# Performance work log

Hardware: AMD Instinct MI355X
Metric: run time of the kernel (lower is better)

Reference implementation:

```python
import jax, jax.numpy as jnp
import numpy as np

N = 100000
D = 64
H = 4 * D  # 256
E = 1000000


def setup_inputs() -> dict:
    key = jax.random.key(0)
    ks = jax.random.split(key, 9)
    return {
        "loc_feat": jax.random.normal(ks[0], (N, D), dtype=jnp.float32),
        "geo_src": jax.random.randint(ks[1], (E,), 0, N),
        "geo_dst": jax.random.randint(ks[2], (E,), 0, N),
        "trans_src": jax.random.randint(ks[3], (E,), 0, N),
        "trans_dst": jax.random.randint(ks[4], (E,), 0, N),
        "trans_w": jax.random.uniform(ks[5], (E,), dtype=jnp.float32),
        "W1": jax.random.normal(ks[6], (D, H), dtype=jnp.float32) * (1.0 / np.sqrt(D)),
        "b1": jax.random.normal(ks[7], (H,), dtype=jnp.float32) * 0.01,
        "W2": jax.random.normal(ks[8], (H, 1), dtype=jnp.float32) * (1.0 / np.sqrt(H)),
    }


def reference(loc_feat, geo_src, geo_dst, trans_src, trans_dst, trans_w, W1, b1, W2):
    n = loc_feat.shape[0]
    # etype 'geo': copy_u + mean  -> segment mean of src features at dst
    geo_sum = jax.ops.segment_sum(loc_feat[geo_src], geo_dst, num_segments=n)
    cnt = jax.ops.segment_sum(jnp.ones(geo_src.shape[0], loc_feat.dtype), geo_dst, num_segments=n)
    geo = jnp.where(cnt[:, None] > 0, geo_sum / jnp.maximum(cnt, 1.0)[:, None], 0.0)
    # etype 'trans': u_mul_e + sum -> weighted segment sum
    trans = jax.ops.segment_sum(loc_feat[trans_src] * trans_w[:, None], trans_dst, num_segments=n)
    # semantic attention fuse over the two relation views
    z = jnp.stack([geo, trans], axis=1)          # [N, 2, D]
    h = jnp.tanh(jnp.einsum('nkd,dh->nkh', z, W1) + b1)  # [N, 2, H]
    w = jnp.einsum('nkh,ho->nko', h, W2).mean(0)  # [2, 1] (mean over nodes)
    beta = jax.nn.softmax(w, axis=0)              # [2, 1]
    return (beta[None, :, :] * z).sum(1)          # [N, D]
```

## Files before the change

kernel.cpp:

```cpp
#include <hip/hip_runtime.h>
#include <hip/hip_bf16.h>

#define N_NODES 100000
#define DIM 64
#define HID 256
#define E_EDGES 1000000
#define TWO_N (2 * N_NODES)
#define MLP_ROWBLOCKS (TWO_N / 64)

#define TILE 240
#define NBINS 417
#define CAP 3072
#define EPB 8192
#define GEO_BLOCKS 123

typedef short short8 __attribute__((ext_vector_type(8)));
typedef float f32x4 __attribute__((ext_vector_type(4)));
typedef unsigned short us4 __attribute__((ext_vector_type(4)));

__device__ __forceinline__ float tanh_fast(float x) {
    x = fminf(fmaxf(x, -15.0f), 15.0f);
    float e = __expf(2.0f * x);
    return (e - 1.0f) / (e + 1.0f);
}

__device__ __forceinline__ unsigned short f2bf(float x) {
    unsigned u = __float_as_uint(x);
    u = u + 0x7FFFu + ((u >> 16) & 1u);
    return (unsigned short)(u >> 16);
}

__device__ __forceinline__ float bf2f(unsigned short u) {
    return __uint_as_float(((unsigned)u) << 16);
}

__global__ void pack_feat_kernel(const float* __restrict__ feat,
                                 unsigned short* __restrict__ fb) {
    int i = blockIdx.x * 256 + threadIdx.x;
    float4 v = ((const float4*)feat)[i];
    us4 o;
    o[0] = f2bf(v.x); o[1] = f2bf(v.y); o[2] = f2bf(v.z); o[3] = f2bf(v.w);
    ((us4*)fb)[i] = o;
}

__global__ void bin_fill_kernel(const int* __restrict__ gs, const int* __restrict__ gd,
                                const int* __restrict__ ts, const int* __restrict__ td,
                                const float* __restrict__ tw,
                                int* __restrict__ gcount,
                                int* __restrict__ gbin, int2* __restrict__ tbin) {
    __shared__ int hist[NBINS];
    __shared__ int baseS[NBINS];
    __shared__ int cur[NBINS];
    int t = threadIdx.x;
    int blk = blockIdx.x;
    int rel = (blk >= GEO_BLOCKS) ? 1 : 0;
    int e0 = (rel ? blk - GEO_BLOCKS : blk) * EPB;
    const int* dstp = rel ? td : gd;
    const int* srcp = rel ? ts : gs;

    for (int i = t; i < NBINS; i += 256) { hist[i] = 0; cur[i] = 0; }
    __syncthreads();

    #pragma unroll
    for (int j = 0; j < EPB / 1024; ++j) {
        int idx = e0 + j * 1024 + 4 * t;
        if (idx + 3 < E_EDGES) {
            int4 v = *(const int4*)&dstp[idx];
            atomicAdd(&hist[v.x / TILE], 1);
            atomicAdd(&hist[v.y / TILE], 1);
            atomicAdd(&hist[v.z / TILE], 1);
            atomicAdd(&hist[v.w / TILE], 1);
        } else {
            for (int i2 = 0; i2 < 4; ++i2)
                if (idx + i2 < E_EDGES) atomicAdd(&hist[dstp[idx + i2] / TILE], 1);
        }
    }
    __syncthreads();

    for (int i = t; i < NBINS; i += 256) {
        int h = hist[i];
        baseS[i] = (h > 0) ? (i * CAP + atomicAdd(&gcount[rel * NBINS + i], h)) : 0;
    }
    __syncthreads();

    if (!rel) {
        #pragma unroll
        for (int j = 0; j < EPB / 1024; ++j) {
            int idx = e0 + j * 1024 + 4 * t;
            bool vec = (idx + 3 < E_EDGES);
            int4 dv, sv;
            if (vec) { dv = *(const int4*)&dstp[idx]; sv = *(const int4*)&srcp[idx]; }
            int dd[4] = {dv.x, dv.y, dv.z, dv.w};
            int ss[4] = {sv.x, sv.y, sv.z, sv.w};
            for (int i2 = 0; i2 < 4; ++i2) {
                if (!vec) {
                    if (idx + i2 >= E_EDGES) continue;
                    dd[i2] = dstp[idx + i2]; ss[i2] = srcp[idx + i2];
                }
                int d = dd[i2];
                int bin = d / TILE;
                int pos = atomicAdd(&cur[bin], 1);
                int gi = baseS[bin] + pos;
                if (gi < (bin + 1) * CAP)
                    gbin[gi] = ss[i2] | ((d - bin * TILE) << 20);
            }
        }
    } else {
        #pragma unroll
        for (int j = 0; j < EPB / 1024; ++j) {
            int idx = e0 + j * 1024 + 4 * t;
            bool vec = (idx + 3 < E_EDGES);
            int4 dv, sv; float4 wv;
            if (vec) {
                dv = *(const int4*)&dstp[idx];
                sv = *(const int4*)&srcp[idx];
                wv = *(const float4*)&tw[idx];
            }
            int dd[4] = {dv.x, dv.y, dv.z, dv.w};
            int ss[4] = {sv.x, sv.y, sv.z, sv.w};
            float ww[4] = {wv.x, wv.y, wv.z, wv.w};
            for (int i2 = 0; i2 < 4; ++i2) {
                if (!vec) {
                    if (idx + i2 >= E_EDGES) continue;
                    dd[i2] = dstp[idx + i2]; ss[i2] = srcp[idx + i2]; ww[i2] = tw[idx + i2];
                }
                int d = dd[i2];
                int bin = d / TILE;
                int pos = atomicAdd(&cur[bin], 1);
                int gi = baseS[bin] + pos;
                if (gi < (bin + 1) * CAP)
                    tbin[gi] = make_int2(ss[i2] | ((d - bin * TILE) << 20),
                                         __float_as_int(ww[i2]));
            }
        }
    }
}

__global__ void __launch_bounds__(512) aggregate_kernel(
        const unsigned short* __restrict__ featb,
        const int* __restrict__ gbin, const int2* __restrict__ tbin,
        const int* __restrict__ gcount,
        unsigned short* __restrict__ zb) {
    __shared__ int   srcS[CAP];
    __shared__ float wS[CAP];
    __shared__ int   histS[TILE];
    __shared__ int   baseS[TILE];
    __shared__ int   curS[TILE];
    __shared__ int   scanS[256];

    int b = blockIdx.x;
    int rel = (b >= NBINS) ? 1 : 0;
    int bin = rel ? b - NBINS : b;
    int node0 = bin * TILE;
    int nNodes = min(TILE, N_NODES - node0);
    int t = threadIdx.x, lane = t & 63, wave = t >> 6;
    int q = lane >> 4, ql = lane & 15;

    int nE = gcount[b];
    if (nE > CAP) nE = CAP;

    for (int i = t; i < TILE; i += 512) histS[i] = 0;
    __syncthreads();

    if (!rel) {
        const int* bp = gbin + (size_t)bin * CAP;
        for (int i = t; i < nE; i += 512) atomicAdd(&histS[bp[i] >> 20], 1);
    } else {
        const int2* bp = tbin + (size_t)bin * CAP;
        for (int i = t; i < nE; i += 512) atomicAdd(&histS[bp[i].x >> 20], 1);
    }
    __syncthreads();

    if (t < 256) scanS[t] = (t < TILE) ? histS[t] : 0;
    __syncthreads();
    #pragma unroll
    for (int off = 1; off < 256; off <<= 1) {
        int add = 0;
        if (t < 256 && t >= off) add = scanS[t - off];
        __syncthreads();
        if (t < 256) scanS[t] += add;
        __syncthreads();
    }
    if (t < TILE) {
        int base = scanS[t] - histS[t];
        baseS[t] = base;
        curS[t] = base;
    }
    __syncthreads();

    if (!rel) {
        const int* bp = gbin + (size_t)bin * CAP;
        for (int i = t; i < nE; i += 512) {
            int p = bp[i];
            int pos = atomicAdd(&curS[p >> 20], 1);
            srcS[pos] = p & 0xFFFFF;
        }
    } else {
        const int2* bp = tbin + (size_t)bin * CAP;
        for (int i = t; i < nE; i += 512) {
            int2 p = bp[i];
            int pos = atomicAdd(&curS[p.x >> 20], 1);
            srcS[pos] = p.x & 0xFFFFF;
            wS[pos] = __int_as_float(p.y);
        }
    }
    __syncthreads();

    for (int nl = wave; nl < nNodes; nl += 8) {
        int deg = histS[nl];
        int base = baseS[nl];
        float a0 = 0.f, a1 = 0.f, a2 = 0.f, a3 = 0.f;
        if (!rel) {
            int k = 0;
            for (; k + 7 < deg; k += 8) {
                int s0 = srcS[base + k + q];
                int s1 = srcS[base + k + 4 + q];
                us4 r0 = *(const us4*)&featb[(size_t)s0 * DIM + ql * 4];
                us4 r1 = *(const us4*)&featb[(size_t)s1 * DIM + ql * 4];
                a0 += bf2f(r0[0]) + bf2f(r1[0]);
                a1 += bf2f(r0[1]) + bf2f(r1[1]);
                a2 += bf2f(r0[2]) + bf2f(r1[2]);
                a3 += bf2f(r0[3]) + bf2f(r1[3]);
            }
            for (; k < deg; k += 4) {
                int e = k + q;
                if (e < deg) {
                    int s = srcS[base + e];
                    us4 r = *(const us4*)&featb[(size_t)s * DIM + ql * 4];
                    a0 += bf2f(r[0]); a1 += bf2f(r[1]);
                    a2 += bf2f(r[2]); a3 += bf2f(r[3]);
                }
            }
        } else {
            int k = 0;
            for (; k + 7 < deg; k += 8) {
                int s0 = srcS[base + k + q];
                int s1 = srcS[base + k + 4 + q];
                float w0 = wS[base + k + q];
                float w1 = wS[base + k + 4 + q];
                us4 r0 = *(const us4*)&featb[(size_t)s0 * DIM + ql * 4];
                us4 r1 = *(const us4*)&featb[(size_t)s1 * DIM + ql * 4];
                a0 += bf2f(r0[0]) * w0 + bf2f(r1[0]) * w1;
                a1 += bf2f(r0[1]) * w0 + bf2f(r1[1]) * w1;
                a2 += bf2f(r0[2]) * w0 + bf2f(r1[2]) * w1;
                a3 += bf2f(r0[3]) * w0 + bf2f(r1[3]) * w1;
            }
            for (; k < deg; k += 4) {
                int e = k + q;
                if (e < deg) {
                    int s = srcS[base + e];
                    float w = wS[base + e];
                    us4 r = *(const us4*)&featb[(size_t)s * DIM + ql * 4];
                    a0 += bf2f(r[0]) * w; a1 += bf2f(r[1]) * w;
                    a2 += bf2f(r[2]) * w; a3 += bf2f(r[3]) * w;
                }
            }
        }
        a0 += __shfl_down(a0, 16); a1 += __shfl_down(a1, 16);
        a2 += __shfl_down(a2, 16); a3 += __shfl_down(a3, 16);
        a0 += __shfl_down(a0, 32); a1 += __shfl_down(a1, 32);
        a2 += __shfl_down(a2, 32); a3 += __shfl_down(a3, 32);
        if (lane < 16) {
            float sc = rel ? 1.0f : 1.0f / fmaxf((float)deg, 1.0f);
            us4 o;
            o[0] = f2bf(a0 * sc); o[1] = f2bf(a1 * sc);
            o[2] = f2bf(a2 * sc); o[3] = f2bf(a3 * sc);
            size_t row = (size_t)(rel ? N_NODES + node0 + nl : node0 + nl);
            *(us4*)&zb[row * DIM + ql * 4] = o;
        }
    }
}

__global__ void pack_w1_kernel(const float* __restrict__ W1, unsigned short* __restrict__ W1p) {
    int i = blockIdx.x * 256 + threadIdx.x;
    int j = i & 7;
    int r = i >> 3;
    int nidx = r & 15; r >>= 4;
    int q = r & 3; r >>= 2;
    int khalf = r & 1;
    int n = r >> 1;
    int k = 32 * khalf + 8 * q + j;
    int c = 16 * n + nidx;
    W1p[i] = f2bf(W1[k * HID + c]);
}

__global__ void __launch_bounds__(256) mlp_mfma_kernel(
        const unsigned short* __restrict__ zb,
        const unsigned short* __restrict__ W1p,
        const float* __restrict__ bias1, const float* __restrict__ W2,
        float* __restrict__ partials) {
    __shared__ float wred[4][2];
    int t = threadIdx.x, lane = t & 63, wave = t >> 6;
    int m = lane & 15, q = lane >> 4;
    int base = blockIdx.x * 64 + wave * 16;
    int R = base + m;

    const unsigned short* rowp = zb + (size_t)R * DIM;
    short8 a0 = *(const short8*)(rowp + q * 8);
    short8 a1 = *(const short8*)(rowp + 32 + q * 8);

    float c0 = 0.0f, c1 = 0.0f;
    const short8* W1v = (const short8*)W1p;

    #pragma unroll 4
    for (int n = 0; n < 16; ++n) {
        short8 b0 = W1v[(n * 2 + 0) * 64 + lane];
        short8 bK = W1v[(n * 2 + 1) * 64 + lane];
        f32x4 acc = {0.0f, 0.0f, 0.0f, 0.0f};
        acc = __builtin_amdgcn_mfma_f32_16x16x32_bf16(a0, b0, acc, 0, 0, 0);
        acc = __builtin_amdgcn_mfma_f32_16x16x32_bf16(a1, bK, acc, 0, 0, 0);
        int col = 16 * n + m;
        float bj = bias1[col];
        float w2 = W2[col];
        #pragma unroll
        for (int reg = 0; reg < 4; ++reg) {
            int Rr = base + q * 4 + reg;
            float h = tanh_fast(acc[reg] + bj);
            float contrib = h * w2;
            if (Rr < N_NODES) c0 += contrib; else c1 += contrib;
        }
    }

    #pragma unroll
    for (int off = 32; off > 0; off >>= 1) {
        c0 += __shfl_down(c0, off);
        c1 += __shfl_down(c1, off);
    }
    if (lane == 0) { wred[wave][0] = c0; wred[wave][1] = c1; }
    __syncthreads();
    if (t == 0) {
        partials[blockIdx.x * 2 + 0] = wred[0][0] + wred[1][0] + wred[2][0] + wred[3][0];
        partials[blockIdx.x * 2 + 1] = wred[0][1] + wred[1][1] + wred[2][1] + wred[3][1];
    }
}

__global__ void beta_kernel(const float* __restrict__ partials, float* __restrict__ beta) {
    __shared__ float wred[4][2];
    int t = threadIdx.x;
    float c0 = 0.0f, c1 = 0.0f;
    for (int i = t; i < MLP_ROWBLOCKS; i += 256) {
        c0 += partials[i * 2 + 0];
        c1 += partials[i * 2 + 1];
    }
    #pragma unroll
    for (int off = 32; off > 0; off >>= 1) {
        c0 += __shfl_down(c0, off);
        c1 += __shfl_down(c1, off);
    }
    int lane = t & 63, wv = t >> 6;
    if (lane == 0) { wred[wv][0] = c0; wred[wv][1] = c1; }
    __syncthreads();
    if (t == 0) {
        float s0 = (wred[0][0] + wred[1][0] + wred[2][0] + wred[3][0]) / (float)N_NODES;
        float s1 = (wred[0][1] + wred[1][1] + wred[2][1] + wred[3][1]) / (float)N_NODES;
        float m = fmaxf(s0, s1);
        float e0 = __expf(s0 - m), e1 = __expf(s1 - m);
        float inv = 1.0f / (e0 + e1);
        beta[0] = e0 * inv;
        beta[1] = e1 * inv;
    }
}

__global__ void combine_kernel(const unsigned short* __restrict__ zb,
                               const float* __restrict__ beta,
                               float* __restrict__ out) {
    int gid = blockIdx.x * 256 + threadIdx.x;
    float b0 = beta[0];
    float b1 = beta[1];
    uint4 g = *(const uint4*)&zb[(size_t)gid * 8];
    uint4 tr = *(const uint4*)&zb[(size_t)N_NODES * DIM + (size_t)gid * 8];
    float4 o0, o1;
    o0.x = b0 * __uint_as_float(g.x << 16) + b1 * __uint_as_float(tr.x << 16);
    o0.y = b0 * __uint_as_float(g.x & 0xFFFF0000u) + b1 * __uint_as_float(tr.x & 0xFFFF0000u);
    o0.z = b0 * __uint_as_float(g.y << 16) + b1 * __uint_as_float(tr.y << 16);
    o0.w = b0 * __uint_as_float(g.y & 0xFFFF0000u) + b1 * __uint_as_float(tr.y & 0xFFFF0000u);
    o1.x = b0 * __uint_as_float(g.z << 16) + b1 * __uint_as_float(tr.z << 16);
    o1.y = b0 * __uint_as_float(g.z & 0xFFFF0000u) + b1 * __uint_as_float(tr.z & 0xFFFF0000u);
    o1.z = b0 * __uint_as_float(g.w << 16) + b1 * __uint_as_float(tr.w << 16);
    o1.w = b0 * __uint_as_float(g.w & 0xFFFF0000u) + b1 * __uint_as_float(tr.w & 0xFFFF0000u);
    *(float4*)&out[(size_t)gid * 8] = o0;
    *(float4*)&out[(size_t)gid * 8 + 4] = o1;
}

extern "C" void kernel_launch(void* const* d_in, const int* in_sizes, int n_in,
                              void* d_out, int out_size, void* d_ws, size_t ws_size,
                              hipStream_t stream) {
    const float* loc_feat = (const float*)d_in[0];
    const int* geo_src    = (const int*)d_in[1];
    const int* geo_dst    = (const int*)d_in[2];
    const int* trans_src  = (const int*)d_in[3];
    const int* trans_dst  = (const int*)d_in[4];
    const float* trans_w  = (const float*)d_in[5];
    const float* W1       = (const float*)d_in[6];
    const float* b1       = (const float*)d_in[7];
    const float* W2       = (const float*)d_in[8];
    float* out = (float*)d_out;

    int*   gcount   = (int*)d_ws;
    int*   gbin     = gcount + 2 * NBINS;
    int2*  tbin     = (int2*)(gbin + (size_t)NBINS * CAP);
    float* partials = (float*)(tbin + (size_t)NBINS * CAP);
    float* beta     = partials + 2 * MLP_ROWBLOCKS;
    unsigned short* W1p   = (unsigned short*)(beta + 2);
    unsigned short* featb = W1p + 16384;
    unsigned short* zb    = featb + (size_t)N_NODES * DIM;

    hipMemsetAsync(gcount, 0, 2 * NBINS * sizeof(int), stream);

    pack_feat_kernel<<<(N_NODES * DIM / 4) / 256, 256, 0, stream>>>(loc_feat, featb);
    pack_w1_kernel<<<64, 256, 0, stream>>>(W1, W1p);
    bin_fill_kernel<<<2 * GEO_BLOCKS, 256, 0, stream>>>(geo_src, geo_dst, trans_src,
                                                        trans_dst, trans_w,
                                                        gcount, gbin, tbin);
    aggregate_kernel<<<2 * NBINS, 512, 0, stream>>>(featb, gbin, tbin, gcount, zb);
    mlp_mfma_kernel<<<MLP_ROWBLOCKS, 256, 0, stream>>>(zb, W1p, b1, W2, partials);
    beta_kernel<<<1, 256, 0, stream>>>(partials, beta);
    combine_kernel<<<(N_NODES * DIM / 8) / 256, 256, 0, stream>>>(zb, beta, out);
}
```

Measured before the change: 247.7 us.

## Halve bin tiles, stage fill through shared-memory sort, one node per quarter-wave

Halves the destination tile to 120 nodes, which doubles the number of bins and aggregate blocks, and lowers per-bin capacity and edges per fill block. The bin fill kernel now loads edges once into registers, builds a local histogram with an exclusive scan, and counting-sorts the edges in shared memory. It then writes them to global bins contiguously, in place of scattered per-edge writes. The aggregate kernel gives each quarter-wave its own node, dropping the cross-quarter shuffle reduction, and unrolls the gather loop by four. The change trades more blocks and more shared memory per fill block for better write coalescing and a more even aggregate load, but lanes within a wave may diverge when node degrees differ, and the smaller capacity raises the risk of bin overflow.

```diff
diff --git a/kernel.cpp b/kernel.cpp
--- a/kernel.cpp
+++ b/kernel.cpp
@@ -8,11 +8,11 @@
 #define TWO_N (2 * N_NODES)
 #define MLP_ROWBLOCKS (TWO_N / 64)
 
-#define TILE 240
-#define NBINS 417
-#define CAP 3072
-#define EPB 8192
-#define GEO_BLOCKS 123
+#define TILE 120
+#define NBINS 834
+#define CAP 1600
+#define EPB 4096
+#define FILL_BLOCKS 245
 
 typedef short short8 __attribute__((ext_vector_type(8)));
 typedef float f32x4 __attribute__((ext_vector_type(4)));
@@ -43,100 +43,116 @@
     ((us4*)fb)[i] = o;
 }
 
-__global__ void bin_fill_kernel(const int* __restrict__ gs, const int* __restrict__ gd,
-                                const int* __restrict__ ts, const int* __restrict__ td,
-                                const float* __restrict__ tw,
-                                int* __restrict__ gcount,
-                                int* __restrict__ gbin, int2* __restrict__ tbin) {
-    __shared__ int hist[NBINS];
-    __shared__ int baseS[NBINS];
-    __shared__ int cur[NBINS];
+__global__ void __launch_bounds__(512) bin_fill_kernel(
+        const int* __restrict__ gs, const int* __restrict__ gd,
+        const int* __restrict__ ts, const int* __restrict__ td,
+        const float* __restrict__ tw,
+        int* __restrict__ gcount,
+        int* __restrict__ gbin, int2* __restrict__ tbin) {
+    __shared__ int   hist[NBINS];
+    __shared__ int   adjS[NBINS];
+    __shared__ int   curS[NBINS];
+    __shared__ int   pS[EPB];
+    __shared__ float w2S[EPB];
+    __shared__ unsigned short binS[EPB];
+    __shared__ int   scanS[512];
+
     int t = threadIdx.x;
     int blk = blockIdx.x;
-    int rel = (blk >= GEO_BLOCKS) ? 1 : 0;
-    int e0 = (rel ? blk - GEO_BLOCKS : blk) * EPB;
+    int rel = (blk >= FILL_BLOCKS) ? 1 : 0;
+    int e0 = (rel ? blk - FILL_BLOCKS : blk) * EPB;
     const int* dstp = rel ? td : gd;
     const int* srcp = rel ? ts : gs;
 
-    for (int i = t; i < NBINS; i += 256) { hist[i] = 0; cur[i] = 0; }
-    __syncthreads();
-
-    #pragma unroll
-    for (int j = 0; j < EPB / 1024; ++j) {
-        int idx = e0 + j * 1024 + 4 * t;
+    for (int i = t; i < NBINS; i += 512) hist[i] = 0;
+    __syncthreads();
+
+    int d_[8], s_[8];
+    float w_[8];
+    #pragma unroll
+    for (int j = 0; j < 2; ++j) {
+        int idx = e0 + j * 2048 + 4 * t;
         if (idx + 3 < E_EDGES) {
-            int4 v = *(const int4*)&dstp[idx];
-            atomicAdd(&hist[v.x / TILE], 1);
-            atomicAdd(&hist[v.y / TILE], 1);
-            atomicAdd(&hist[v.z / TILE], 1);
-            atomicAdd(&hist[v.w / TILE], 1);
+            int4 dv = *(const int4*)&dstp[idx];
+            int4 sv = *(const int4*)&srcp[idx];
+            d_[4*j+0] = dv.x; d_[4*j+1] = dv.y; d_[4*j+2] = dv.z; d_[4*j+3] = dv.w;
+            s_[4*j+0] = sv.x; s_[4*j+1] = sv.y; s_[4*j+2] = sv.z; s_[4*j+3] = sv.w;
+            if (rel) {
+                float4 wv = *(const float4*)&tw[idx];
+                w_[4*j+0] = wv.x; w_[4*j+1] = wv.y; w_[4*j+2] = wv.z; w_[4*j+3] = wv.w;
+            }
         } else {
-            for (int i2 = 0; i2 < 4; ++i2)
-                if (idx + i2 < E_EDGES) atomicAdd(&hist[dstp[idx + i2] / TILE], 1);
-        }
-    }
-    __syncthreads();
-
-    for (int i = t; i < NBINS; i += 256) {
-        int h = hist[i];
-        baseS[i] = (h > 0) ? (i * CAP + atomicAdd(&gcount[rel * NBINS + i], h)) : 0;
-    }
-    __syncthreads();
-
+            #pragma unroll
+            for (int i2 = 0; i2 < 4; ++i2) {
+                bool ok = (idx + i2 < E_EDGES);
+                d_[4*j+i2] = ok ? dstp[idx + i2] : -1;
+                s_[4*j+i2] = ok ? srcp[idx + i2] : 0;
+                w_[4*j+i2] = (ok && rel) ? tw[idx + i2] : 0.0f;
+            }
+        }
+    }
+    #pragma unroll
+    for (int i = 0; i < 8; ++i)
+        if (d_[i] >= 0) atomicAdd(&hist[d_[i] / TILE], 1);
+    __syncthreads();
+
+    int carry = 0;
+    for (int cb = 0; cb < NBINS; cb += 512) {
+        int i = cb + t;
+        int c = (i < NBINS) ? hist[i] : 0;
+        __syncthreads();
+        scanS[t] = c;
+        __syncthreads();
+        int v = c;
+        #pragma unroll
+        for (int off = 1; off < 512; off <<= 1) {
+            int add = (t >= off) ? scanS[t - off] : 0;
+            __syncthreads();
+            v += add;
+            scanS[t] = v;
+            __syncthreads();
+        }
+        if (i < NBINS) {
+            int lb = v - c + carry;
+            curS[i] = lb;
+            int gb = (c > 0) ? (i * CAP + atomicAdd(&gcount[rel * NBINS + i], c)) : 0;
+            adjS[i] = gb - lb;
+        }
+        carry += scanS[511];
+    }
+    __syncthreads();
+
+    #pragma unroll
+    for (int i = 0; i < 8; ++i) {
+        int d = d_[i];
+        if (d < 0) continue;
+        int bin = d / TILE;
+        int pos = atomicAdd(&curS[bin], 1);
+        pS[pos] = s_[i] | ((d - bin * TILE) << 20);
+        binS[pos] = (unsigned short)bin;
+        if (rel) w2S[pos] = w_[i];
+    }
+    __syncthreads();
+
+    int nV = min(EPB, E_EDGES - e0);
     if (!rel) {
-        #pragma unroll
-        for (int j = 0; j < EPB / 1024; ++j) {
-            int idx = e0 + j * 1024 + 4 * t;
-            bool vec = (idx + 3 < E_EDGES);
-            int4 dv, sv;
-            if (vec) { dv = *(const int4*)&dstp[idx]; sv = *(const int4*)&srcp[idx]; }
-            int dd[4] = {dv.x, dv.y, dv.z, dv.w};
-            int ss[4] = {sv.x, sv.y, sv.z, sv.w};
-            for (int i2 = 0; i2 < 4; ++i2) {
-                if (!vec) {
-                    if (idx + i2 >= E_EDGES) continue;
-                    dd[i2] = dstp[idx + i2]; ss[i2] = srcp[idx + i2];
-                }
-                int d = dd[i2];
-                int bin = d / TILE;
-                int pos = atomicAdd(&cur[bin], 1);
-                int gi = baseS[bin] + pos;
-                if (gi < (bin + 1) * CAP)
-                    gbin[gi] = ss[i2] | ((d - bin * TILE) << 20);
-            }
+        for (int i = t; i < nV; i += 512) {
+            int b = binS[i];
+            int gi = adjS[b] + i;
+            if (gi < (b + 1) * CAP)
+                gbin[gi] = pS[i];
         }
     } else {
-        #pragma unroll
-        for (int j = 0; j < EPB / 1024; ++j) {
-            int idx = e0 + j * 1024 + 4 * t;
-            bool vec = (idx + 3 < E_EDGES);
-            int4 dv, sv; float4 wv;
-            if (vec) {
-                dv = *(const int4*)&dstp[idx];
-                sv = *(const int4*)&srcp[idx];
-                wv = *(const float4*)&tw[idx];
-            }
-            int dd[4] = {dv.x, dv.y, dv.z, dv.w};
-            int ss[4] = {sv.x, sv.y, sv.z, sv.w};
-            float ww[4] = {wv.x, wv.y, wv.z, wv.w};
-            for (int i2 = 0; i2 < 4; ++i2) {
-                if (!vec) {
-                    if (idx + i2 >= E_EDGES) continue;
-                    dd[i2] = dstp[idx + i2]; ss[i2] = srcp[idx + i2]; ww[i2] = tw[idx + i2];
-                }
-                int d = dd[i2];
-                int bin = d / TILE;
-                int pos = atomicAdd(&cur[bin], 1);
-                int gi = baseS[bin] + pos;
-                if (gi < (bin + 1) * CAP)
-                    tbin[gi] = make_int2(ss[i2] | ((d - bin * TILE) << 20),
-                                         __float_as_int(ww[i2]));
-            }
-        }
-    }
-}
-
-__global__ void __launch_bounds__(512) aggregate_kernel(
+        for (int i = t; i < nV; i += 512) {
+            int b = binS[i];
+            int gi = adjS[b] + i;
+            if (gi < (b + 1) * CAP)
+                tbin[gi] = make_int2(pS[i], __float_as_int(w2S[i]));
+        }
+    }
+}
+
+__global__ void __launch_bounds__(256) aggregate_kernel(
         const unsigned short* __restrict__ featb,
         const int* __restrict__ gbin, const int2* __restrict__ tbin,
         const int* __restrict__ gcount,
@@ -146,7 +162,7 @@
     __shared__ int   histS[TILE];
     __shared__ int   baseS[TILE];
     __shared__ int   curS[TILE];
-    __shared__ int   scanS[256];
+    __shared__ int   scanS[128];
 
     int b = blockIdx.x;
     int rel = (b >= NBINS) ? 1 : 0;
@@ -159,26 +175,26 @@
     int nE = gcount[b];
     if (nE > CAP) nE = CAP;
 
-    for (int i = t; i < TILE; i += 512) histS[i] = 0;
+    for (int i = t; i < TILE; i += 256) histS[i] = 0;
     __syncthreads();
 
     if (!rel) {
         const int* bp = gbin + (size_t)bin * CAP;
-        for (int i = t; i < nE; i += 512) atomicAdd(&histS[bp[i] >> 20], 1);
+        for (int i = t; i < nE; i += 256) atomicAdd(&histS[bp[i] >> 20], 1);
     } else {
         const int2* bp = tbin + (size_t)bin * CAP;
-        for (int i = t; i < nE; i += 512) atomicAdd(&histS[bp[i].x >> 20], 1);
-    }
-    __syncthreads();
-
-    if (t < 256) scanS[t] = (t < TILE) ? histS[t] : 0;
-    __syncthreads();
-    #pragma unroll
-    for (int off = 1; off < 256; off <<= 1) {
+        for (int i = t; i < nE; i += 256) atomicAdd(&histS[bp[i].x >> 20], 1);
+    }
+    __syncthreads();
+
+    if (t < 128) scanS[t] = (t < TILE) ? histS[t] : 0;
+    __syncthreads();
+    #pragma unroll
+    for (int off = 1; off < 128; off <<= 1) {
         int add = 0;
-        if (t < 256 && t >= off) add = scanS[t - off];
+        if (t < 128 && t >= off) add = scanS[t - off];
         __syncthreads();
-        if (t < 256) scanS[t] += add;
+        if (t < 128) scanS[t] += add;
         __syncthreads();
     }
     if (t < TILE) {
@@ -190,14 +206,14 @@
 
     if (!rel) {
         const int* bp = gbin + (size_t)bin * CAP;
-        for (int i = t; i < nE; i += 512) {
+        for (int i = t; i < nE; i += 256) {
             int p = bp[i];
             int pos = atomicAdd(&curS[p >> 20], 1);
             srcS[pos] = p & 0xFFFFF;
         }
     } else {
         const int2* bp = tbin + (size_t)bin * CAP;
-        for (int i = t; i < nE; i += 512) {
+        for (int i = t; i < nE; i += 256) {
             int2 p = bp[i];
             int pos = atomicAdd(&curS[p.x >> 20], 1);
             srcS[pos] = p.x & 0xFFFFF;
@@ -206,61 +222,57 @@
     }
     __syncthreads();
 
-    for (int nl = wave; nl < nNodes; nl += 8) {
-        int deg = histS[nl];
-        int base = baseS[nl];
+    for (int nl0 = wave * 4; nl0 < nNodes; nl0 += 16) {
+        int nl = nl0 + q;
+        bool act = (nl < nNodes);
+        int deg = act ? histS[nl] : 0;
+        int base = act ? baseS[nl] : 0;
         float a0 = 0.f, a1 = 0.f, a2 = 0.f, a3 = 0.f;
         if (!rel) {
             int k = 0;
-            for (; k + 7 < deg; k += 8) {
-                int s0 = srcS[base + k + q];
-                int s1 = srcS[base + k + 4 + q];
+            for (; k + 3 < deg; k += 4) {
+                int s0 = srcS[base + k], s1 = srcS[base + k + 1];
+                int s2 = srcS[base + k + 2], s3 = srcS[base + k + 3];
                 us4 r0 = *(const us4*)&featb[(size_t)s0 * DIM + ql * 4];
                 us4 r1 = *(const us4*)&featb[(size_t)s1 * DIM + ql * 4];
-                a0 += bf2f(r0[0]) + bf2f(r1[0]);
-                a1 += bf2f(r0[1]) + bf2f(r1[1]);
-                a2 += bf2f(r0[2]) + bf2f(r1[2]);
-                a3 += bf2f(r0[3]) + bf2f(r1[3]);
-            }
-            for (; k < deg; k += 4) {
-                int e = k + q;
-                if (e < deg) {
-                    int s = srcS[base + e];
-                    us4 r = *(const us4*)&featb[(size_t)s * DIM + ql * 4];
-                    a0 += bf2f(r[0]); a1 += bf2f(r[1]);
-                    a2 += bf2f(r[2]); a3 += bf2f(r[3]);
-                }
+                us4 r2 = *(const us4*)&featb[(size_t)s2 * DIM + ql * 4];
+                us4 r3 = *(const us4*)&featb[(size_t)s3 * DIM + ql * 4];
+                a0 += (bf2f(r0[0]) + bf2f(r1[0])) + (bf2f(r2[0]) + bf2f(r3[0]));
+                a1 += (bf2f(r0[1]) + bf2f(r1[1])) + (bf2f(r2[1]) + bf2f(r3[1]));
+                a2 += (bf2f(r0[2]) + bf2f(r1[2])) + (bf2f(r2[2]) + bf2f(r3[2]));
+                a3 += (bf2f(r0[3]) + bf2f(r1[3])) + (bf2f(r2[3]) + bf2f(r3[3]));
+            }
+            for (; k < deg; ++k) {
+                int s = srcS[base + k];
+                us4 r = *(const us4*)&featb[(size_t)s * DIM + ql * 4];
+                a0 += bf2f(r[0]); a1 += bf2f(r[1]);
+                a2 += bf2f(r[2]); a3 += bf2f(r[3]);
             }
         } else {
             int k = 0;
-            for (; k + 7 < deg; k += 8) {
-                int s0 = srcS[base + k + q];
-                int s1 = srcS[base + k + 4 + q];
-                float w0 = wS[base + k + q];
-                float w1 = wS[base + k + 4 + q];
+            for (; k + 3 < deg; k += 4) {
+                int s0 = srcS[base + k], s1 = srcS[base + k + 1];
+                int s2 = srcS[base + k + 2], s3 = srcS[base + k + 3];
+                float w0 = wS[base + k], w1 = wS[base + k + 1];
+                float w2 = wS[base + k + 2], w3 = wS[base + k + 3];
                 us4 r0 = *(const us4*)&featb[(size_t)s0 * DIM + ql * 4];
                 us4 r1 = *(const us4*)&featb[(size_t)s1 * DIM + ql * 4];
-                a0 += bf2f(r0[0]) * w0 + bf2f(r1[0]) * w1;
-                a1 += bf2f(r0[1]) * w0 + bf2f(r1[1]) * w1;
-                a2 += bf2f(r0[2]) * w0 + bf2f(r1[2]) * w1;
-                a3 += bf2f(r0[3]) * w0 + bf2f(r1[3]) * w1;
-            }
-            for (; k < deg; k += 4) {
-                int e = k + q;
-                if (e < deg) {
-                    int s = srcS[base + e];
-                    float w = wS[base + e];
-                    us4 r = *(const us4*)&featb[(size_t)s * DIM + ql * 4];
-                    a0 += bf2f(r[0]) * w; a1 += bf2f(r[1]) * w;
-                    a2 += bf2f(r[2]) * w; a3 += bf2f(r[3]) * w;
-                }
-            }
-        }
-        a0 += __shfl_down(a0, 16); a1 += __shfl_down(a1, 16);
-        a2 += __shfl_down(a2, 16); a3 += __shfl_down(a3, 16);
-        a0 += __shfl_down(a0, 32); a1 += __shfl_down(a1, 32);
-        a2 += __shfl_down(a2, 32); a3 += __shfl_down(a3, 32);
-        if (lane < 16) {
+                us4 r2 = *(const us4*)&featb[(size_t)s2 * DIM + ql * 4];
+                us4 r3 = *(const us4*)&featb[(size_t)s3 * DIM + ql * 4];
+                a0 += (bf2f(r0[0]) * w0 + bf2f(r1[0]) * w1) + (bf2f(r2[0]) * w2 + bf2f(r3[0]) * w3);
+                a1 += (bf2f(r0[1]) * w0 + bf2f(r1[1]) * w1) + (bf2f(r2[1]) * w2 + bf2f(r3[1]) * w3);
+                a2 += (bf2f(r0[2]) * w0 + bf2f(r1[2]) * w1) + (bf2f(r2[2]) * w2 + bf2f(r3[2]) * w3);
+                a3 += (bf2f(r0[3]) * w0 + bf2f(r1[3]) * w1) + (bf2f(r2[3]) * w2 + bf2f(r3[3]) * w3);
+            }
+            for (; k < deg; ++k) {
+                int s = srcS[base + k];
+                float w = wS[base + k];
+                us4 r = *(const us4*)&featb[(size_t)s * DIM + ql * 4];
+                a0 += bf2f(r[0]) * w; a1 += bf2f(r[1]) * w;
+                a2 += bf2f(r[2]) * w; a3 += bf2f(r[3]) * w;
+            }
+        }
+        if (act) {
             float sc = rel ? 1.0f : 1.0f / fmaxf((float)deg, 1.0f);
             us4 o;
             o[0] = f2bf(a0 * sc); o[1] = f2bf(a1 * sc);
@@ -409,10 +421,10 @@
 
     pack_feat_kernel<<<(N_NODES * DIM / 4) / 256, 256, 0, stream>>>(loc_feat, featb);
     pack_w1_kernel<<<64, 256, 0, stream>>>(W1, W1p);
-    bin_fill_kernel<<<2 * GEO_BLOCKS, 256, 0, stream>>>(geo_src, geo_dst, trans_src,
-                                                        trans_dst, trans_w,
-                                                        gcount, gbin, tbin);
-    aggregate_kernel<<<2 * NBINS, 512, 0, stream>>>(featb, gbin, tbin, gcount, zb);
+    bin_fill_kernel<<<2 * FILL_BLOCKS, 512, 0, stream>>>(geo_src, geo_dst, trans_src,
+                                                         trans_dst, trans_w,
+                                                         gcount, gbin, tbin);
+    aggregate_kernel<<<2 * NBINS, 256, 0, stream>>>(featb, gbin, tbin, gcount, zb);
     mlp_mfma_kernel<<<MLP_ROWBLOCKS, 256, 0, stream>>>(zb, W1p, b1, W2, partials);
     beta_kernel<<<1, 256, 0, stream>>>(partials, beta);
     combine_kernel<<<(N_NODES * DIM / 8) / 256, 256, 0, stream>>>(zb, beta, out);
```

New measurement: 233.9 us. 5.6% less time.
